# Optimization experiments

Measured on AMD Instinct MI355X. Metric: run time of the kernel, lower is better.

Reference implementation:

```python
import jax, jax.numpy as jnp
import numpy as np

N, E, H, FE, FV, L, FL, FO = 20000, 320000, 256, 64, 64, 4, 1024, 1


def setup_inputs() -> dict:
    key = jax.random.key(0)
    ks = jax.random.split(key, 28)
    s = 0.05
    rn = lambda k, shp: jax.random.normal(k, shp, jnp.float32) * s
    inp = {
        'x': jax.random.normal(ks[0], (N, FV), jnp.float32),
        'edge_attr': jax.random.normal(ks[1], (E, FE), jnp.float32),
        'edge_index': jax.random.randint(ks[2], (2, E), 0, N, jnp.int64) if False else jax.random.randint(ks[2], (2, E), 0, N),
        'ew': rn(ks[3], (H, FE)), 'eb': rn(ks[4], (H,)),
        'vw': rn(ks[5], (H, FV)), 'vb': rn(ks[6], (H,)),
        'Le_w': rn(ks[7], (L, H, H)), 'Le_b': rn(ks[8], (L, H)),
        'Lv_w': rn(ks[9], (L, H, H)), 'Lv_b': rn(ks[10], (L, H)),
        'bne_g': jnp.ones((L, H), jnp.float32), 'bne_b': jnp.zeros((L, H), jnp.float32),
        'bnv_g': jnp.ones((L, H), jnp.float32), 'bnv_b': jnp.zeros((L, H), jnp.float32),
        'gru_wih': rn(ks[11], (L, 3 * H, H)), 'gru_whh': rn(ks[12], (L, 3 * H, H)),
        'gru_bih': rn(ks[13], (L, 3 * H)), 'gru_bhh': rn(ks[14], (L, 3 * H)),
        'fin_w': rn(ks[15], (FL, H)), 'fin_b': rn(ks[16], (FL,)),
        'out_w': rn(ks[17], (FO, FL)), 'out_b': rn(ks[18], (FO,)),
    }
    return inp


def _bn(x, g, b):
    # BatchNorm1d, training-mode batch statistics (biased variance), eps=1e-5
    m = x.mean(axis=0)
    v = x.var(axis=0)
    return (x - m) * jax.lax.rsqrt(v + 1e-5) * g + b


def _forward(x, edge_attr, edge_index, ew, eb, vw, vb, Le_w, Le_b, Lv_w, Lv_b,
             bne_g, bne_b, bnv_g, bnv_b, gru_wih, gru_whh, gru_bih, gru_bhh,
             fin_w, fin_b, out_w, out_b):
    n_nodes = x.shape[0]
    num_layers = Le_w.shape[0]
    src, dst = edge_index[0], edge_index[1]
    seg = jnp.concatenate([src, dst])  # each edge contributes to both endpoints
    e_in = edge_attr @ ew.T + eb       # [E, H]
    v_in = x @ vw.T + vb               # [N, H]
    for k in range(num_layers):
        e = e_in @ Le_w[k].T + Le_b[k]
        vp = v_in @ Lv_w[k].T + Lv_b[k]
        ep = jax.nn.relu(_bn(e + vp[src] + vp[dst], bne_g[k], bne_b[k]))  # [E, H]
        # scatter-max of incident edge features into each vertex
        vie = jax.ops.segment_max(jnp.concatenate([ep, ep], axis=0), seg,
                                  num_segments=n_nodes)
        vie = jnp.where(jnp.isfinite(vie), vie, 0.0)  # isolated vertices -> 0
        # single-step GRU: input vie, hidden v_in
        gi = vie @ gru_wih[k].T + gru_bih[k]
        gh = v_in @ gru_whh[k].T + gru_bhh[k]
        ir, iz, ig = jnp.split(gi, 3, axis=1)
        hr, hz, hg = jnp.split(gh, 3, axis=1)
        r = jax.nn.sigmoid(ir + hr)
        z = jax.nn.sigmoid(iz + hz)
        n = jnp.tanh(ig + r * hg)
        h = (1.0 - z) * n + z * v_in
        v_c = jax.nn.relu(_bn(h, bnv_g[k], bnv_b[k]))
        v_in = v_c + v_in
        e_in = ep + e_in
    e_fin = e_in @ fin_w.T + fin_b
    return e_fin @ out_w.T + out_b  # [E, 1]


def reference(x, edge_attr, edge_index, ew, eb, vw, vb, Le_w, Le_b, Lv_w, Lv_b,
              bne_g, bne_b, bnv_g, bnv_b, gru_wih, gru_whh, gru_bih, gru_bhh,
              fin_w, fin_b, out_w, out_b):
    return _forward(x, edge_attr, edge_index, ew, eb, vw, vb, Le_w, Le_b, Lv_w,
                    Lv_b, bne_g, bne_b, bnv_g, bnv_b, gru_wih, gru_whh,
                    gru_bih, gru_bhh, fin_w, fin_b, out_w, out_b)
```

## Files before the change

kernel.cpp:

```cpp
#include <hip/hip_runtime.h>
#include <stdint.h>

constexpr int N  = 20000;
constexpr int E  = 320000;
constexpr int H  = 256;
constexpr int FEAT = 64;
constexpr int NL = 4;
constexpr int FL = 1024;
constexpr int NB_E = E / 64;

typedef unsigned short u16;
typedef short bf16x8 __attribute__((ext_vector_type(8)));
typedef float f32x4 __attribute__((ext_vector_type(4)));

__device__ __forceinline__ float bf2f(u16 u) {
    union { uint32_t i; float f; } v; v.i = ((uint32_t)u) << 16; return v.f;
}
__device__ __forceinline__ u16 f2bf(float f) {
    union { uint32_t i; float f; } v; v.f = f;
    uint32_t r = v.i + 0x7FFFu + ((v.i >> 16) & 1u);
    return (u16)(r >> 16);
}
__device__ __forceinline__ float sigmf(float x) { return 1.f / (1.f + __expf(-x)); }
__device__ __forceinline__ float tanhf_(float x) { return 2.f / (1.f + __expf(-2.f * x)) - 1.f; }

__device__ __forceinline__ unsigned int encf(float x) {
    unsigned int u = __float_as_uint(x);
    return (u & 0x80000000u) ? ~u : (u | 0x80000000u);
}
__device__ __forceinline__ float decf(unsigned int k) {
    unsigned int u = (k & 0x80000000u) ? (k ^ 0x80000000u) : ~k;
    return __uint_as_float(u);
}
__device__ __forceinline__ bf16x8 addbf8(bf16x8 a, bf16x8 b) {
    bf16x8 o;
#pragma unroll
    for (int j = 0; j < 8; ++j)
        o[j] = (short)f2bf(bf2f((u16)(unsigned short)a[j]) + bf2f((u16)(unsigned short)b[j]));
    return o;
}

template <bool W16>
__device__ __forceinline__ bf16x8 ldb(const u16* wb, const float* wf, size_t off) {
    if constexpr (W16) {
        return *(const bf16x8*)(wb + off);
    } else {
        float4 b0 = *(const float4*)(wf + off);
        float4 b1 = *(const float4*)(wf + off + 4);
        bf16x8 r;
        r[0] = (short)f2bf(b0.x); r[1] = (short)f2bf(b0.y);
        r[2] = (short)f2bf(b0.z); r[3] = (short)f2bf(b0.w);
        r[4] = (short)f2bf(b1.x); r[5] = (short)f2bf(b1.y);
        r[6] = (short)f2bf(b1.z); r[7] = (short)f2bf(b1.w);
        return r;
    }
}

__global__ void k_fuse_final(const float* __restrict__ fin_w, const float* __restrict__ fin_b,
                             const float* __restrict__ out_w, const float* __restrict__ out_b,
                             float* __restrict__ w_fo) {
    int h = threadIdx.x;
    float acc = 0.f;
    for (int f = 0; f < FL; ++f) acc = fmaf(out_w[f], fin_w[(size_t)f * H + h], acc);
    w_fo[h] = acc;
    if (h == 0) {
        float b = 0.f;
        for (int f = 0; f < FL; ++f) b = fmaf(out_w[f], fin_b[f], b);
        w_fo[H] = b + out_b[0];
    }
}

__global__ void k_cvt_w(const float* __restrict__ w, u16* __restrict__ o, int n4) {
    int i = blockIdx.x * 256 + threadIdx.x;
    if (i < n4) {
        float4 v = *(const float4*)(w + (size_t)i * 4);
        *(ushort4*)(o + (size_t)i * 4) = make_ushort4(f2bf(v.x), f2bf(v.y), f2bf(v.z), f2bf(v.w));
    }
}

__global__ void k_cvt_w_sw(const float* __restrict__ w, u16* __restrict__ o, int total) {
    int i = blockIdx.x * 256 + threadIdx.x;
    if (i >= total) return;
    int l16 = i & 15;
    int qd  = (i >> 4) & 3;
    int ks  = (i >> 6) & 7;
    int g   = (i >> 9) & 15;
    int ly  = i >> 13;
    int row = g * 16 + l16;
    int k   = ks * 32 + qd * 8;
    const float* src = w + ((size_t)ly * H + row) * H + k;
    u16* dst = o + (size_t)i * 8;
    *(ushort4*)dst       = make_ushort4(f2bf(src[0]), f2bf(src[1]), f2bf(src[2]), f2bf(src[3]));
    *(ushort4*)(dst + 4) = make_ushort4(f2bf(src[4]), f2bf(src[5]), f2bf(src[6]), f2bf(src[7]));
}

__global__ void k_zero_int(int* __restrict__ p, int n) {
    int i = blockIdx.x * 256 + threadIdx.x;
    if (i < n) p[i] = 0;
}
__global__ void k_zero_f64(double* __restrict__ p, int n) {
    int i = blockIdx.x * 256 + threadIdx.x;
    if (i < n) p[i] = 0.0;
}
__global__ void k_hist2(const int* __restrict__ src, const int* __restrict__ dst,
                        int* __restrict__ curS, int* __restrict__ curD) {
    int e = blockIdx.x * 256 + threadIdx.x;
    if (e < E) { atomicAdd(&curS[src[e]], 1); atomicAdd(&curD[dst[e]], 1); }
}
__global__ void k_scan(int* __restrict__ cur) {
    __shared__ int cs[256];
    int t = threadIdx.x;
    constexpr int CH = (N + 255) / 256;
    int beg = t * CH, end = min(beg + CH, N);
    int s = 0;
    for (int i = beg; i < end; ++i) s += cur[i];
    cs[t] = s;
    __syncthreads();
    for (int off = 1; off < 256; off <<= 1) {
        int v = cs[t];
        int u = (t >= off) ? cs[t - off] : 0;
        __syncthreads();
        cs[t] = v + u;
        __syncthreads();
    }
    int run = (t > 0) ? cs[t - 1] : 0;
    for (int i = beg; i < end; ++i) { int d = cur[i]; cur[i] = run; run += d; }
}
__global__ void k_fill_perm(const int* __restrict__ src, const int* __restrict__ dst,
                            int* __restrict__ curS, int* __restrict__ curD,
                            int4* __restrict__ adjS, int4* __restrict__ sd2, int* __restrict__ pos) {
    int e = blockIdx.x * 256 + threadIdx.x;
    if (e < E) {
        int s = src[e], d = dst[e];
        int q = atomicAdd(&curD[d], 1);
        sd2[q] = make_int4(s, d, e, 0);
        pos[e] = q;
        int p = atomicAdd(&curS[s], 1);
        adjS[p] = make_int4(q, s, d, s);
    }
}
__global__ void k_fill_u32(unsigned int* __restrict__ p, unsigned int val) {
    size_t i = ((size_t)blockIdx.x * 256 + threadIdx.x) * 4;
    uint4 v = make_uint4(val, val, val, val);
    *(uint4*)(p + i) = v;
}

template <bool W16>
__global__ __launch_bounds__(256, 3) void k_proj_mfma(
    const float* __restrict__ A, const u16* __restrict__ wb, const float* __restrict__ wf,
    const float* __restrict__ bias, u16* __restrict__ C, int M, const int* __restrict__ perm)
{
    __shared__ u16 As[64][72];
    int t = threadIdx.x;
    int row0 = blockIdx.x * 64;
    int r = t >> 2, q = t & 3;
    if (row0 + r < M) {
        const float* gp = A + (size_t)(row0 + r) * FEAT + q * 16;
#pragma unroll
        for (int i = 0; i < 4; ++i) {
            float4 v = *(const float4*)(gp + i * 4);
            *(ushort4*)&As[r][q * 16 + i * 4] = make_ushort4(f2bf(v.x), f2bf(v.y), f2bf(v.z), f2bf(v.w));
        }
    } else {
#pragma unroll
        for (int i = 0; i < 4; ++i) *(ushort4*)&As[r][q * 16 + i * 4] = make_ushort4(0, 0, 0, 0);
    }
    __syncthreads();
    int w = t >> 6, l = t & 63, lane16 = l & 15, quad = l >> 4;
    f32x4 acc[4][4];
#pragma unroll
    for (int i = 0; i < 4; ++i)
#pragma unroll
        for (int j = 0; j < 4; ++j) acc[i][j] = (f32x4){0.f, 0.f, 0.f, 0.f};
#pragma unroll
    for (int k0 = 0; k0 < FEAT; k0 += 32) {
        bf16x8 a[4], b[4];
#pragma unroll
        for (int mt = 0; mt < 4; ++mt)
            a[mt] = *(const bf16x8*)&As[mt * 16 + lane16][k0 + quad * 8];
#pragma unroll
        for (int nt = 0; nt < 4; ++nt)
            b[nt] = ldb<W16>(wb, wf, (size_t)(w * 16 + nt * 64 + lane16) * FEAT + k0 + quad * 8);
#pragma unroll
        for (int mt = 0; mt < 4; ++mt)
#pragma unroll
            for (int nt = 0; nt < 4; ++nt)
                acc[mt][nt] = __builtin_amdgcn_mfma_f32_16x16x32_bf16(a[mt], b[nt], acc[mt][nt], 0, 0, 0);
    }
#pragma unroll
    for (int nt = 0; nt < 4; ++nt) {
        int col = w * 16 + nt * 64 + lane16;
        float bv = bias[col];
#pragma unroll
        for (int mt = 0; mt < 4; ++mt)
#pragma unroll
            for (int reg = 0; reg < 4; ++reg) {
                int row = mt * 16 + quad * 4 + reg;
                if (row0 + row < M) {
                    int pr = perm ? perm[row0 + row] : row0 + row;
                    C[(size_t)pr * H + col] = f2bf(acc[mt][nt][reg] + bv);
                }
            }
    }
}

template <bool W16>
__global__ __launch_bounds__(256, 2) void k_node_mfma(
    const u16* __restrict__ A, const u16* __restrict__ wb, const float* __restrict__ wf,
    u16* __restrict__ C)
{
    __shared__ u16 As[64][264];
    int t = threadIdx.x;
    int row0 = blockIdx.x * 64;
    int rows = min(64, N - row0);
    int r = t >> 2, q = t & 3;
    if (r < rows) {
        const u16* gp = A + (size_t)(row0 + r) * H + q * 64;
#pragma unroll
        for (int i = 0; i < 16; ++i)
            *(ushort4*)&As[r][q * 64 + i * 4] = *(const ushort4*)(gp + i * 4);
    } else {
#pragma unroll
        for (int i = 0; i < 16; ++i) *(ushort4*)&As[r][q * 64 + i * 4] = make_ushort4(0, 0, 0, 0);
    }
    __syncthreads();
    int w = t >> 6, l = t & 63, lane16 = l & 15, quad = l >> 4;
    f32x4 acc[4][4];
#pragma unroll
    for (int i = 0; i < 4; ++i)
#pragma unroll
        for (int j = 0; j < 4; ++j) acc[i][j] = (f32x4){0.f, 0.f, 0.f, 0.f};
    for (int k0 = 0; k0 < H; k0 += 32) {
        bf16x8 a[4], b[4];
#pragma unroll
        for (int mt = 0; mt < 4; ++mt)
            a[mt] = *(const bf16x8*)&As[mt * 16 + lane16][k0 + quad * 8];
#pragma unroll
        for (int nt = 0; nt < 4; ++nt)
            b[nt] = ldb<W16>(wb, wf, (size_t)(w * 16 + nt * 64 + lane16) * H + k0 + quad * 8);
#pragma unroll
        for (int mt = 0; mt < 4; ++mt)
#pragma unroll
            for (int nt = 0; nt < 4; ++nt)
                acc[mt][nt] = __builtin_amdgcn_mfma_f32_16x16x32_bf16(a[mt], b[nt], acc[mt][nt], 0, 0, 0);
    }
#pragma unroll
    for (int nt = 0; nt < 4; ++nt) {
        int col = w * 16 + nt * 64 + lane16;
#pragma unroll
        for (int mt = 0; mt < 4; ++mt)
#pragma unroll
            for (int reg = 0; reg < 4; ++reg) {
                int row = mt * 16 + quad * 4 + reg;
                if (row < rows)
                    C[(size_t)(row0 + row) * H + col] = f2bf(acc[mt][nt][reg]);
            }
    }
}

__global__ __launch_bounds__(512, 4) void k_edge_first(
    const u16* __restrict__ ein2, const u16* __restrict__ wsw,
    const u16* __restrict__ vp, const int4* __restrict__ sd2,
    const int* __restrict__ endo,
    unsigned int* __restrict__ vie, double* __restrict__ stats_e)
{
    __shared__ u16 As[64][264];
    __shared__ u16 Us[64][264];
    __shared__ int s_node[64];
    __shared__ int s_int[64];
    u16 (*praw)[264] = As;

    int t = threadIdx.x;
    int p0 = blockIdx.x * 64;
    int r = t >> 3, q = t & 7;
    {
        int4 en = sd2[p0 + r];
        const u16* gp = ein2 + (size_t)(p0 + r) * H + q * 32;
        const u16* vs = vp + (size_t)en.x * H + q * 32;
        const u16* vd = vp + (size_t)en.y * H + q * 32;
#pragma unroll
        for (int i = 0; i < 4; ++i)
            *(bf16x8*)&As[r][q * 32 + i * 8] = *(const bf16x8*)(gp + i * 8);
#pragma unroll
        for (int i = 0; i < 4; ++i) {
            bf16x8 a8 = *(const bf16x8*)(vs + i * 8);
            bf16x8 b8 = *(const bf16x8*)(vd + i * 8);
            *(bf16x8*)&Us[r][q * 32 + i * 8] = addbf8(a8, b8);
        }
    }
    if (t < 64) {
        int nd = sd2[p0 + t].y;
        s_node[t] = nd;
        int seg0 = p0 + (t & 32);
        int st = (nd == 0) ? 0 : endo[nd - 1];
        int ee = endo[nd];
        s_int[t] = (st >= seg0) && (ee <= seg0 + 32);
    }
    __syncthreads();

    int w = t >> 6, l = t & 63, lane16 = l & 15, quad = l >> 4;
    f32x4 acc[4][2];
#pragma unroll
    for (int i = 0; i < 4; ++i)
#pragma unroll
        for (int j = 0; j < 2; ++j) acc[i][j] = (f32x4){0.f, 0.f, 0.f, 0.f};
    int woff = (quad * 16 + lane16) * 8;
    for (int ks = 0; ks < 8; ++ks) {
        int k0 = ks * 32;
        bf16x8 a[4], b[2];
#pragma unroll
        for (int mt = 0; mt < 4; ++mt)
            a[mt] = *(const bf16x8*)&As[mt * 16 + lane16][k0 + quad * 8];
#pragma unroll
        for (int nt = 0; nt < 2; ++nt)
            b[nt] = *(const bf16x8*)(wsw + (size_t)(w * 2 + nt) * 4096 + ks * 512 + woff);
#pragma unroll
        for (int mt = 0; mt < 4; ++mt)
#pragma unroll
            for (int nt = 0; nt < 2; ++nt)
                acc[mt][nt] = __builtin_amdgcn_mfma_f32_16x16x32_bf16(a[mt], b[nt], acc[mt][nt], 0, 0, 0);
    }
    __syncthreads();

#pragma unroll
    for (int nt = 0; nt < 2; ++nt) {
        int col = w * 32 + nt * 16 + lane16;
        float s = 0.f, qq = 0.f;
#pragma unroll
        for (int mt = 0; mt < 4; ++mt)
#pragma unroll
            for (int reg = 0; reg < 4; ++reg) {
                int row = mt * 16 + quad * 4 + reg;
                float v = acc[mt][nt][reg] + bf2f(Us[row][col]);
                praw[row][col] = f2bf(v);
                s += v; qq += v * v;
            }
        s  += __shfl_xor(s, 16, 64);  s  += __shfl_xor(s, 32, 64);
        qq += __shfl_xor(qq, 16, 64); qq += __shfl_xor(qq, 32, 64);
        if (quad == 0) {
            int slice = blockIdx.x & 63;
            atomicAdd(&stats_e[(size_t)slice * 512 + col], (double)s);
            atomicAdd(&stats_e[(size_t)slice * 512 + 256 + col], (double)qq);
        }
    }
    __syncthreads();
    {
        int seg = t >> 8, col = t & 255;
        int base = seg * 32;
        int cur = s_node[base];
        float m = bf2f(praw[base][col]);
        for (int rr = 1; rr < 32; ++rr) {
            int nd = s_node[base + rr];
            float v = bf2f(praw[base + rr][col]);
            if (nd != cur) {
                if (s_int[base + rr - 1]) vie[(size_t)cur * H + col] = encf(m);
                else atomicMax(&vie[(size_t)cur * H + col], encf(m));
                cur = nd; m = v;
            } else m = fmaxf(m, v);
        }
        if (s_int[base + 31]) vie[(size_t)cur * H + col] = encf(m);
        else atomicMax(&vie[(size_t)cur * H + col], encf(m));
    }
}

__global__ __launch_bounds__(512, 4) void k_edge_second(
    const u16* __restrict__ ein2, const u16* __restrict__ wsw,
    const u16* __restrict__ vp, const int4* __restrict__ adj,
    unsigned int* __restrict__ vie,
    const float* __restrict__ scale, const float* __restrict__ shift,
    u16* __restrict__ ein_rw)
{
    __shared__ u16 As[64][264];
    __shared__ u16 Us[64][264];
    __shared__ int s_pos[64];
    __shared__ int s_node[64];
    u16 (*praw)[264] = As;

    int t = threadIdx.x;
    int p0 = blockIdx.x * 64;
    int r = t >> 3, q = t & 7;
    {
        int4 en = adj[p0 + r];
        const u16* gp = ein2 + (size_t)en.x * H + q * 32;
        const u16* vs = vp + (size_t)en.y * H + q * 32;
        const u16* vd = vp + (size_t)en.z * H + q * 32;
#pragma unroll
        for (int i = 0; i < 4; ++i)
            *(bf16x8*)&As[r][q * 32 + i * 8] = *(const bf16x8*)(gp + i * 8);
#pragma unroll
        for (int i = 0; i < 4; ++i) {
            bf16x8 a8 = *(const bf16x8*)(vs + i * 8);
            bf16x8 b8 = *(const bf16x8*)(vd + i * 8);
            *(bf16x8*)&Us[r][q * 32 + i * 8] = addbf8(a8, b8);
        }
    }
    if (t < 64) {
        int4 en = adj[p0 + t];
        s_pos[t] = en.x; s_node[t] = en.w;
    }
    __syncthreads();

    int w = t >> 6, l = t & 63, lane16 = l & 15, quad = l >> 4;
    f32x4 acc[4][2];
#pragma unroll
    for (int i = 0; i < 4; ++i)
#pragma unroll
        for (int j = 0; j < 2; ++j) acc[i][j] = (f32x4){0.f, 0.f, 0.f, 0.f};
    int woff = (quad * 16 + lane16) * 8;
    for (int ks = 0; ks < 8; ++ks) {
        int k0 = ks * 32;
        bf16x8 a[4], b[2];
#pragma unroll
        for (int mt = 0; mt < 4; ++mt)
            a[mt] = *(const bf16x8*)&As[mt * 16 + lane16][k0 + quad * 8];
#pragma unroll
        for (int nt = 0; nt < 2; ++nt)
            b[nt] = *(const bf16x8*)(wsw + (size_t)(w * 2 + nt) * 4096 + ks * 512 + woff);
#pragma unroll
        for (int mt = 0; mt < 4; ++mt)
#pragma unroll
            for (int nt = 0; nt < 2; ++nt)
                acc[mt][nt] = __builtin_amdgcn_mfma_f32_16x16x32_bf16(a[mt], b[nt], acc[mt][nt], 0, 0, 0);
    }
    __syncthreads();

#pragma unroll
    for (int nt = 0; nt < 2; ++nt) {
        int col = w * 32 + nt * 16 + lane16;
#pragma unroll
        for (int mt = 0; mt < 4; ++mt)
#pragma unroll
            for (int reg = 0; reg < 4; ++reg) {
                int row = mt * 16 + quad * 4 + reg;
                praw[row][col] = f2bf(acc[mt][nt][reg] + bf2f(Us[row][col]));
            }
    }
    __syncthreads();
    {
        int seg = t >> 8, col = t & 255;
        int base = seg * 32;
        int cur = s_node[base];
        float m = bf2f(praw[base][col]);
        for (int rr = 1; rr < 32; ++rr) {
            int nd = s_node[base + rr];
            float v = bf2f(praw[base + rr][col]);
            if (nd != cur) {
                atomicMax(&vie[(size_t)cur * H + col], encf(m));
                cur = nd; m = v;
            } else m = fmaxf(m, v);
        }
        atomicMax(&vie[(size_t)cur * H + col], encf(m));
    }
    {
        u16* gp = ein_rw + (size_t)s_pos[r] * H + q * 32;
        const float* scp = scale + q * 32;
        const float* shp = shift + q * 32;
#pragma unroll
        for (int i = 0; i < 8; ++i) {
            int c = q * 32 + i * 4;
            ushort2 pa = *(const ushort2*)&praw[r][c];
            ushort2 pb = *(const ushort2*)&praw[r][c + 2];
            float4 sc = *(const float4*)(scp + i * 4);
            float4 sh = *(const float4*)(shp + i * 4);
            ushort4 ev = *(const ushort4*)(gp + i * 4);
            float o0 = bf2f(ev.x) + fmaxf(fmaf(bf2f(pa.x), sc.x, sh.x), 0.f);
            float o1 = bf2f(ev.y) + fmaxf(fmaf(bf2f(pa.y), sc.y, sh.y), 0.f);
            float o2 = bf2f(ev.z) + fmaxf(fmaf(bf2f(pb.x), sc.z, sh.z), 0.f);
            float o3 = bf2f(ev.w) + fmaxf(fmaf(bf2f(pb.y), sc.w, sh.w), 0.f);
            *(ushort4*)(gp + i * 4) = make_ushort4(f2bf(o0), f2bf(o1), f2bf(o2), f2bf(o3));
        }
    }
}

__global__ void k_bn_final_e(const double* __restrict__ stats_e,
                             const float* __restrict__ g, const float* __restrict__ b,
                             float* __restrict__ scale, float* __restrict__ shift) {
    int j = threadIdx.x;
    double m = 0.0, q = 0.0;
    for (int s = 0; s < 64; ++s) {
        m += stats_e[(size_t)s * 512 + j];
        q += stats_e[(size_t)s * 512 + 256 + j];
    }
    m /= (double)E;
    double var = q / (double)E - m * m;
    if (var < 0.0) var = 0.0;
    float inv = rsqrtf((float)var + 1e-5f);
    float sc = g[j] * inv;
    scale[j] = sc;
    shift[j] = b[j] - (float)m * sc;
}

__global__ void k_bn_final(const double* __restrict__ stats, int base,
                           const float* __restrict__ g, const float* __restrict__ b,
                           double cnt, float* __restrict__ scale, float* __restrict__ shift) {
    int j = threadIdx.x;
    double m = stats[base + j] / cnt;
    double var = stats[base + 256 + j] / cnt - m * m;
    if (var < 0.0) var = 0.0;
    float inv = rsqrtf((float)var + 1e-5f);
    float sc = g[j] * inv;
    scale[j] = sc;
    shift[j] = b[j] - (float)m * sc;
}

__global__ void k_vie_final(unsigned int* __restrict__ vie_u,
                            const float* __restrict__ scale, const float* __restrict__ shift) {
    size_t idx = ((size_t)blockIdx.x * 256 + threadIdx.x) * 4;
    int col = (int)(idx & (size_t)(H - 1));
    uint4 u = *(const uint4*)(vie_u + idx);
    float4 sc = *(const float4*)(scale + col);
    float4 sh = *(const float4*)(shift + col);
    float4 o;
    o.x = (u.x == 0u) ? 0.f : fmaxf(fmaf(decf(u.x), sc.x, sh.x), 0.f);
    o.y = (u.y == 0u) ? 0.f : fmaxf(fmaf(decf(u.y), sc.y, sh.y), 0.f);
    o.z = (u.z == 0u) ? 0.f : fmaxf(fmaf(decf(u.z), sc.z, sh.z), 0.f);
    o.w = (u.w == 0u) ? 0.f : fmaxf(fmaf(decf(u.w), sc.w, sh.w), 0.f);
    *(float4*)((float*)vie_u + idx) = o;
}

template <bool W16>
__global__ __launch_bounds__(256, 3) void k_gru_mfma(
    const float* __restrict__ vie, const u16* __restrict__ vin,
    const u16* __restrict__ wihb, const float* __restrict__ wihf,
    const u16* __restrict__ whhb, const float* __restrict__ whhf,
    const float* __restrict__ bih, const float* __restrict__ bhh,
    u16* __restrict__ hout, double* __restrict__ stats_v)
{
    __shared__ u16 Ae[32][264];
    __shared__ u16 Av[32][264];
    __shared__ float csum[256], csq[256];
    int t = threadIdx.x;
    int row0 = blockIdx.x * 32;
    int rows = min(32, N - row0);
    int r = t >> 3, q = t & 7;
    if (r < rows) {
        const float* gp = vie + (size_t)(row0 + r) * H + q * 32;
        const u16* hp = vin + (size_t)(row0 + r) * H + q * 32;
#pragma unroll
        for (int i = 0; i < 8; ++i) {
            float4 v = *(const float4*)(gp + i * 4);
            *(ushort4*)&Ae[r][q * 32 + i * 4] = make_ushort4(f2bf(v.x), f2bf(v.y), f2bf(v.z), f2bf(v.w));
        }
#pragma unroll
        for (int i = 0; i < 4; ++i)
            *(bf16x8*)&Av[r][q * 32 + i * 8] = *(const bf16x8*)(hp + i * 8);
    } else {
#pragma unroll
        for (int i = 0; i < 8; ++i) {
            *(ushort4*)&Ae[r][q * 32 + i * 4] = make_ushort4(0, 0, 0, 0);
            *(ushort4*)&Av[r][q * 32 + i * 4] = make_ushort4(0, 0, 0, 0);
        }
    }
    __syncthreads();
    int w = t >> 6, l = t & 63, lane16 = l & 15, quad = l >> 4;

    for (int g = 0; g < 4; ++g) {
        int j = g * 64 + w * 16 + lane16;
        f32x4 aR[2], aZ[2], aIG[2], aHG[2];
#pragma unroll
        for (int mt = 0; mt < 2; ++mt) {
            aR[mt] = (f32x4){0.f, 0.f, 0.f, 0.f};  aZ[mt] = (f32x4){0.f, 0.f, 0.f, 0.f};
            aIG[mt] = (f32x4){0.f, 0.f, 0.f, 0.f}; aHG[mt] = (f32x4){0.f, 0.f, 0.f, 0.f};
        }
        for (int k0 = 0; k0 < H; k0 += 32) {
            size_t kq = (size_t)k0 + quad * 8;
            bf16x8 ae[2], av[2];
#pragma unroll
            for (int mt = 0; mt < 2; ++mt) {
                ae[mt] = *(const bf16x8*)&Ae[mt * 16 + lane16][k0 + quad * 8];
                av[mt] = *(const bf16x8*)&Av[mt * 16 + lane16][k0 + quad * 8];
            }
            bf16x8 bri = ldb<W16>(wihb, wihf, (size_t)j * H + kq);
            bf16x8 bzi = ldb<W16>(wihb, wihf, (size_t)(H + j) * H + kq);
            bf16x8 bgi = ldb<W16>(wihb, wihf, (size_t)(2 * H + j) * H + kq);
            bf16x8 brh = ldb<W16>(whhb, whhf, (size_t)j * H + kq);
            bf16x8 bzh = ldb<W16>(whhb, whhf, (size_t)(H + j) * H + kq);
            bf16x8 bgh = ldb<W16>(whhb, whhf, (size_t)(2 * H + j) * H + kq);
#pragma unroll
            for (int mt = 0; mt < 2; ++mt) {
                aR[mt]  = __builtin_amdgcn_mfma_f32_16x16x32_bf16(ae[mt], bri, aR[mt], 0, 0, 0);
                aR[mt]  = __builtin_amdgcn_mfma_f32_16x16x32_bf16(av[mt], brh, aR[mt], 0, 0, 0);
                aZ[mt]  = __builtin_amdgcn_mfma_f32_16x16x32_bf16(ae[mt], bzi, aZ[mt], 0, 0, 0);
                aZ[mt]  = __builtin_amdgcn_mfma_f32_16x16x32_bf16(av[mt], bzh, aZ[mt], 0, 0, 0);
                aIG[mt] = __builtin_amdgcn_mfma_f32_16x16x32_bf16(ae[mt], bgi, aIG[mt], 0, 0, 0);
                aHG[mt] = __builtin_amdgcn_mfma_f32_16x16x32_bf16(av[mt], bgh, aHG[mt], 0, 0, 0);
            }
        }
        float br_ = bih[j] + bhh[j];
        float bz_ = bih[H + j] + bhh[H + j];
        float bgi_ = bih[2 * H + j];
        float bgh_ = bhh[2 * H + j];
        float s = 0.f, qq = 0.f;
#pragma unroll
        for (int mt = 0; mt < 2; ++mt)
#pragma unroll
            for (int reg = 0; reg < 4; ++reg) {
                int row = mt * 16 + quad * 4 + reg;
                float rr = sigmf(aR[mt][reg] + br_);
                float zz = sigmf(aZ[mt][reg] + bz_);
                float nn = tanhf_(aIG[mt][reg] + bgi_ + rr * (aHG[mt][reg] + bgh_));
                float vv = bf2f(Av[row][j]);
                float hv = (1.f - zz) * nn + zz * vv;
                if (row < rows) {
                    hout[(size_t)(row0 + row) * H + j] = f2bf(hv);
                    s += hv; qq += hv * hv;
                }
            }
        s  += __shfl_xor(s, 16, 64);  s  += __shfl_xor(s, 32, 64);
        qq += __shfl_xor(qq, 16, 64); qq += __shfl_xor(qq, 32, 64);
        if (quad == 0) { csum[j] = s; csq[j] = qq; }
    }
    __syncthreads();
    atomicAdd(&stats_v[t], (double)csum[t]);
    atomicAdd(&stats_v[256 + t], (double)csq[t]);
}

__global__ void k_vertex_update(u16* __restrict__ vin, const u16* __restrict__ h,
                                const float* __restrict__ scale, const float* __restrict__ shift) {
    size_t idx = ((size_t)blockIdx.x * 256 + threadIdx.x) * 4;
    int col = (int)(idx & (size_t)(H - 1));
    ushort4 hv = *(const ushort4*)(h + idx);
    float4 sc = *(const float4*)(scale + col);
    float4 sh = *(const float4*)(shift + col);
    ushort4 vv = *(const ushort4*)(vin + idx);
    float o0 = bf2f(vv.x) + fmaxf(fmaf(bf2f(hv.x), sc.x, sh.x), 0.f);
    float o1 = bf2f(vv.y) + fmaxf(fmaf(bf2f(hv.y), sc.y, sh.y), 0.f);
    float o2 = bf2f(vv.z) + fmaxf(fmaf(bf2f(hv.z), sc.z, sh.z), 0.f);
    float o3 = bf2f(vv.w) + fmaxf(fmaf(bf2f(hv.w), sc.w, sh.w), 0.f);
    *(ushort4*)(vin + idx) = make_ushort4(f2bf(o0), f2bf(o1), f2bf(o2), f2bf(o3));
}

__global__ __launch_bounds__(256) void k_final(const u16* __restrict__ ein2,
                                               const int4* __restrict__ sd2,
                                               const float* __restrict__ w_fo, float* __restrict__ out) {
    int t = threadIdx.x;
    int lane = t & 63;
    int w = (blockIdx.x << 2) + (t >> 6);
    float4 wv = *(const float4*)(w_fo + lane * 4);
    float bfo = w_fo[H];
    int p0 = w * 64;
    for (int p = p0; p < p0 + 64; ++p) {
        ushort4 u = *(const ushort4*)(ein2 + (size_t)p * H + lane * 4);
        float s = bf2f(u.x) * wv.x + bf2f(u.y) * wv.y + bf2f(u.z) * wv.z + bf2f(u.w) * wv.w;
        for (int off = 32; off > 0; off >>= 1) s += __shfl_down(s, off, 64);
        if (lane == 0) out[sd2[p].z] = s + bfo;
    }
}

template <bool W16>
static void run_all(void* const* d_in, void* d_out, void* d_ws, hipStream_t stream) {
    const float* x         = (const float*)d_in[0];
    const float* edge_attr = (const float*)d_in[1];
    const int*   ei        = (const int*)d_in[2];
    const int*   src = ei;
    const int*   dst = ei + E;
    const float* ew  = (const float*)d_in[3];
    const float* eb  = (const float*)d_in[4];
    const float* vw  = (const float*)d_in[5];
    const float* vb  = (const float*)d_in[6];
    const float* Le_w = (const float*)d_in[7];
    const float* Lv_w = (const float*)d_in[9];
    const float* bne_g = (const float*)d_in[11];
    const float* bne_b = (const float*)d_in[12];
    const float* bnv_g = (const float*)d_in[13];
    const float* bnv_b = (const float*)d_in[14];
    const float* gwih  = (const float*)d_in[15];
    const float* gwhh  = (const float*)d_in[16];
    const float* gbih  = (const float*)d_in[17];
    const float* gbhh  = (const float*)d_in[18];
    const float* fin_w = (const float*)d_in[19];
    const float* fin_b = (const float*)d_in[20];
    const float* out_w = (const float*)d_in[21];
    const float* out_b = (const float*)d_in[22];
    float* out = (float*)d_out;

    const size_t nh = (size_t)N * H, eh = (size_t)E * H;
    char* base = (char*)d_ws;
    size_t off = 0;
    auto alloc = [&](size_t bytes) -> char* {
        char* p = base + off;
        off = (off + bytes + 255) & ~(size_t)255;
        return p;
    };
    float* w_fo = (float*)alloc((H + 1) * sizeof(float));
    u16* v_in = (u16*)alloc(nh * sizeof(u16));
    u16* vp   = (u16*)alloc(nh * sizeof(u16));
    unsigned int* vie_u = (unsigned int*)alloc(nh * sizeof(unsigned int));
    u16* e_in = (u16*)alloc(eh * sizeof(u16));
    u16* wbf  = (u16*)alloc((size_t)NL * H * H * sizeof(u16));
    double* stats_e = (double*)alloc((size_t)64 * 512 * sizeof(double));
    double* stats_v = (double*)alloc(512 * sizeof(double));
    float* scale_e = (float*)alloc(H * sizeof(float));
    float* shift_e = (float*)alloc(H * sizeof(float));
    float* scale_v = (float*)alloc(H * sizeof(float));
    float* shift_v = (float*)alloc(H * sizeof(float));
    int* curS = (int*)alloc((size_t)N * sizeof(int));
    int* curD = (int*)alloc((size_t)N * sizeof(int));
    int4* adjS = (int4*)alloc((size_t)E * sizeof(int4));
    int4* sd2  = (int4*)alloc((size_t)E * sizeof(int4));
    int*  pos  = (int*)alloc((size_t)E * sizeof(int));
    u16 *wbf_v = nullptr, *wbf_ih = nullptr, *wbf_hh = nullptr, *ew_b = nullptr, *vw_b = nullptr;
    if (W16) {
        wbf_v  = (u16*)alloc((size_t)NL * H * H * sizeof(u16));
        wbf_ih = (u16*)alloc((size_t)NL * 3 * H * H * sizeof(u16));
        wbf_hh = (u16*)alloc((size_t)NL * 3 * H * H * sizeof(u16));
        ew_b   = (u16*)alloc((size_t)H * FEAT * sizeof(u16));
        vw_b   = (u16*)alloc((size_t)H * FEAT * sizeof(u16));
    }
    u16* hbuf = vp;

    k_fuse_final<<<1, 256, 0, stream>>>(fin_w, fin_b, out_w, out_b, w_fo);
    k_cvt_w_sw<<<(NL * H * H / 8 + 255) / 256, 256, 0, stream>>>(Le_w, wbf, NL * H * H / 8);
    if (W16) {
        k_cvt_w<<<(NL * H * H / 4 + 255) / 256, 256, 0, stream>>>(Lv_w, wbf_v, NL * H * H / 4);
        k_cvt_w<<<(NL * 3 * H * H / 4 + 255) / 256, 256, 0, stream>>>(gwih, wbf_ih, NL * 3 * H * H / 4);
        k_cvt_w<<<(NL * 3 * H * H / 4 + 255) / 256, 256, 0, stream>>>(gwhh, wbf_hh, NL * 3 * H * H / 4);
        k_cvt_w<<<(H * FEAT / 4 + 255) / 256, 256, 0, stream>>>(ew, ew_b, H * FEAT / 4);
        k_cvt_w<<<(H * FEAT / 4 + 255) / 256, 256, 0, stream>>>(vw, vw_b, H * FEAT / 4);
    }
    k_zero_int<<<(N + 255) / 256, 256, 0, stream>>>(curS, N);
    k_zero_int<<<(N + 255) / 256, 256, 0, stream>>>(curD, N);
    k_hist2<<<E / 256, 256, 0, stream>>>(src, dst, curS, curD);
    k_scan<<<1, 256, 0, stream>>>(curS);
    k_scan<<<1, 256, 0, stream>>>(curD);
    k_fill_perm<<<E / 256, 256, 0, stream>>>(src, dst, curS, curD, adjS, sd2, pos);
    const int ntile = (N + 63) / 64;
    k_proj_mfma<W16><<<ntile, 256, 0, stream>>>(x, vw_b, vw, vb, v_in, N, nullptr);
    k_proj_mfma<W16><<<E / 64, 256, 0, stream>>>(edge_attr, ew_b, ew, eb, e_in, E, pos);

    const int nstat = 64 * 512 + 512;
    const int gtile = (N + 31) / 32;
    for (int k = 0; k < NL; ++k) {
        k_zero_f64<<<(nstat + 255) / 256, 256, 0, stream>>>(stats_e, nstat);
        k_fill_u32<<<(int)(nh / 4 / 256), 256, 0, stream>>>(vie_u, 0u);
        k_node_mfma<W16><<<ntile, 256, 0, stream>>>(v_in,
            W16 ? wbf_v + (size_t)k * H * H : nullptr, Lv_w + (size_t)k * H * H, vp);
        k_edge_first<<<NB_E, 512, 0, stream>>>(e_in, wbf + (size_t)k * H * H, vp,
                                               sd2, curD, vie_u, stats_e);
        k_bn_final_e<<<1, 256, 0, stream>>>(stats_e, bne_g + k * H, bne_b + k * H, scale_e, shift_e);
        k_edge_second<<<NB_E, 512, 0, stream>>>(e_in, wbf + (size_t)k * H * H, vp,
                                                adjS, vie_u, scale_e, shift_e, e_in);
        k_vie_final<<<(int)(nh / 4 / 256), 256, 0, stream>>>(vie_u, scale_e, shift_e);
        k_gru_mfma<W16><<<gtile, 256, 0, stream>>>((const float*)vie_u, v_in,
            W16 ? wbf_ih + (size_t)k * 3 * H * H : nullptr, gwih + (size_t)k * 3 * H * H,
            W16 ? wbf_hh + (size_t)k * 3 * H * H : nullptr, gwhh + (size_t)k * 3 * H * H,
            gbih + (size_t)k * 3 * H, gbhh + (size_t)k * 3 * H, hbuf, stats_v);
        k_bn_final<<<1, 256, 0, stream>>>(stats_v, 0, bnv_g + k * H, bnv_b + k * H, (double)N, scale_v, shift_v);
        k_vertex_update<<<(int)(nh / 4 / 256), 256, 0, stream>>>(v_in, hbuf, scale_v, shift_v);
    }
    k_final<<<E / 256, 256, 0, stream>>>(e_in, sd2, w_fo, out);
}

extern "C" void kernel_launch(void* const* d_in, const int* in_sizes, int n_in,
                              void* d_out, int out_size, void* d_ws, size_t ws_size,
                              hipStream_t stream) {
    (void)in_sizes; (void)n_in; (void)out_size;
    const size_t nh = (size_t)N * H, eh = (size_t)E * H;
    auto rup = [](size_t x) { return (x + 255) & ~(size_t)255; };
    size_t need_base = rup((H + 1) * 4) + 2 * rup(nh * 2) + rup(nh * 4) + rup(eh * 2)
                     + rup((size_t)NL * H * H * 2) + rup((size_t)64 * 512 * 8) + rup(512 * 8)
                     + 4 * rup(H * 4) + 2 * rup((size_t)N * 4) + 2 * rup((size_t)E * 16)
                     + rup((size_t)E * 4);
    size_t need_w16 = rup((size_t)NL * H * H * 2)
                    + 2 * rup((size_t)NL * 3 * H * H * 2) + 2 * rup((size_t)H * FEAT * 2);
    if (ws_size == 0 || ws_size >= need_base + need_w16)
        run_all<true>(d_in, d_out, d_ws, stream);
    else
        run_all<false>(d_in, d_out, d_ws, stream);
}
```

Before: 2.444 ms.

## Pre-swizzle all bf16 weights into MFMA fragment order for coalesced loads

Result: no change. 2.467 ms (median of 3 runs) (+1.0%).

```diff
diff --git a/kernel.cpp b/kernel.cpp
--- a/kernel.cpp
+++ b/kernel.cpp
@@ -40,20 +40,15 @@
     return o;
 }
 
-template <bool W16>
-__device__ __forceinline__ bf16x8 ldb(const u16* wb, const float* wf, size_t off) {
-    if constexpr (W16) {
-        return *(const bf16x8*)(wb + off);
-    } else {
-        float4 b0 = *(const float4*)(wf + off);
-        float4 b1 = *(const float4*)(wf + off + 4);
-        bf16x8 r;
-        r[0] = (short)f2bf(b0.x); r[1] = (short)f2bf(b0.y);
-        r[2] = (short)f2bf(b0.z); r[3] = (short)f2bf(b0.w);
-        r[4] = (short)f2bf(b1.x); r[5] = (short)f2bf(b1.y);
-        r[6] = (short)f2bf(b1.z); r[7] = (short)f2bf(b1.w);
-        return r;
-    }
+__device__ __forceinline__ bf16x8 ldbf(const float* wf, size_t off) {
+    float4 b0 = *(const float4*)(wf + off);
+    float4 b1 = *(const float4*)(wf + off + 4);
+    bf16x8 r;
+    r[0] = (short)f2bf(b0.x); r[1] = (short)f2bf(b0.y);
+    r[2] = (short)f2bf(b0.z); r[3] = (short)f2bf(b0.w);
+    r[4] = (short)f2bf(b1.x); r[5] = (short)f2bf(b1.y);
+    r[6] = (short)f2bf(b1.z); r[7] = (short)f2bf(b1.w);
+    return r;
 }
 
 __global__ void k_fuse_final(const float* __restrict__ fin_w, const float* __restrict__ fin_b,
@@ -70,25 +65,18 @@
     }
 }
 
-__global__ void k_cvt_w(const float* __restrict__ w, u16* __restrict__ o, int n4) {
-    int i = blockIdx.x * 256 + threadIdx.x;
-    if (i < n4) {
-        float4 v = *(const float4*)(w + (size_t)i * 4);
-        *(ushort4*)(o + (size_t)i * 4) = make_ushort4(f2bf(v.x), f2bf(v.y), f2bf(v.z), f2bf(v.w));
-    }
-}
-
-__global__ void k_cvt_w_sw(const float* __restrict__ w, u16* __restrict__ o, int total) {
+__global__ void k_cvt_frag(const float* __restrict__ w, u16* __restrict__ o,
+                           int R, int K, int total) {
     int i = blockIdx.x * 256 + threadIdx.x;
     if (i >= total) return;
-    int l16 = i & 15;
-    int qd  = (i >> 4) & 3;
-    int ks  = (i >> 6) & 7;
-    int g   = (i >> 9) & 15;
-    int ly  = i >> 13;
-    int row = g * 16 + l16;
-    int k   = ks * 32 + qd * 8;
-    const float* src = w + ((size_t)ly * H + row) * H + k;
+    int fpm = (R * K) >> 3;
+    int m = i / fpm, f = i % fpm;
+    int l16 = f & 15, qd = (f >> 4) & 3;
+    int rem = f >> 6;
+    int kdiv = K >> 5;
+    int ks = rem % kdiv, g = rem / kdiv;
+    int row = g * 16 + l16, k = ks * 32 + qd * 8;
+    const float* src = w + ((size_t)m * R + row) * K + k;
     u16* dst = o + (size_t)i * 8;
     *(ushort4*)dst       = make_ushort4(f2bf(src[0]), f2bf(src[1]), f2bf(src[2]), f2bf(src[3]));
     *(ushort4*)(dst + 4) = make_ushort4(f2bf(src[4]), f2bf(src[5]), f2bf(src[6]), f2bf(src[7]));
@@ -172,15 +160,21 @@
     for (int i = 0; i < 4; ++i)
 #pragma unroll
         for (int j = 0; j < 4; ++j) acc[i][j] = (f32x4){0.f, 0.f, 0.f, 0.f};
+    int foff = (quad * 16 + lane16) * 8;
 #pragma unroll
     for (int k0 = 0; k0 < FEAT; k0 += 32) {
+        int ks = k0 >> 5;
         bf16x8 a[4], b[4];
 #pragma unroll
         for (int mt = 0; mt < 4; ++mt)
             a[mt] = *(const bf16x8*)&As[mt * 16 + lane16][k0 + quad * 8];
 #pragma unroll
-        for (int nt = 0; nt < 4; ++nt)
-            b[nt] = ldb<W16>(wb, wf, (size_t)(w * 16 + nt * 64 + lane16) * FEAT + k0 + quad * 8);
+        for (int nt = 0; nt < 4; ++nt) {
+            if constexpr (W16)
+                b[nt] = *(const bf16x8*)(wb + (size_t)((nt * 4 + w) * 2 + ks) * 512 + foff);
+            else
+                b[nt] = ldbf(wf, (size_t)(w * 16 + nt * 64 + lane16) * FEAT + k0 + quad * 8);
+        }
 #pragma unroll
         for (int mt = 0; mt < 4; ++mt)
 #pragma unroll
@@ -217,8 +211,8 @@
     if (r < rows) {
         const u16* gp = A + (size_t)(row0 + r) * H + q * 64;
 #pragma unroll
-        for (int i = 0; i < 16; ++i)
-            *(ushort4*)&As[r][q * 64 + i * 4] = *(const ushort4*)(gp + i * 4);
+        for (int i = 0; i < 8; ++i)
+            *(bf16x8*)&As[r][q * 64 + i * 8] = *(const bf16x8*)(gp + i * 8);
     } else {
 #pragma unroll
         for (int i = 0; i < 16; ++i) *(ushort4*)&As[r][q * 64 + i * 4] = make_ushort4(0, 0, 0, 0);
@@ -230,14 +224,20 @@
     for (int i = 0; i < 4; ++i)
 #pragma unroll
         for (int j = 0; j < 4; ++j) acc[i][j] = (f32x4){0.f, 0.f, 0.f, 0.f};
+    int foff = (quad * 16 + lane16) * 8;
     for (int k0 = 0; k0 < H; k0 += 32) {
+        int ks = k0 >> 5;
         bf16x8 a[4], b[4];
 #pragma unroll
         for (int mt = 0; mt < 4; ++mt)
             a[mt] = *(const bf16x8*)&As[mt * 16 + lane16][k0 + quad * 8];
 #pragma unroll
-        for (int nt = 0; nt < 4; ++nt)
-            b[nt] = ldb<W16>(wb, wf, (size_t)(w * 16 + nt * 64 + lane16) * H + k0 + quad * 8);
+        for (int nt = 0; nt < 4; ++nt) {
+            if constexpr (W16)
+                b[nt] = *(const bf16x8*)(wb + (size_t)((nt * 4 + w) * 8 + ks) * 512 + foff);
+            else
+                b[nt] = ldbf(wf, (size_t)(w * 16 + nt * 64 + lane16) * H + k0 + quad * 8);
+        }
 #pragma unroll
         for (int mt = 0; mt < 4; ++mt)
 #pragma unroll
@@ -379,14 +379,17 @@
     int t = threadIdx.x;
     int p0 = blockIdx.x * 64;
     int r = t >> 3, q = t & 7;
+    bf16x8 ein_reg[4];
     {
         int4 en = adj[p0 + r];
         const u16* gp = ein2 + (size_t)en.x * H + q * 32;
         const u16* vs = vp + (size_t)en.y * H + q * 32;
         const u16* vd = vp + (size_t)en.z * H + q * 32;
 #pragma unroll
-        for (int i = 0; i < 4; ++i)
-            *(bf16x8*)&As[r][q * 32 + i * 8] = *(const bf16x8*)(gp + i * 8);
+        for (int i = 0; i < 4; ++i) {
+            ein_reg[i] = *(const bf16x8*)(gp + i * 8);
+            *(bf16x8*)&As[r][q * 32 + i * 8] = ein_reg[i];
+        }
 #pragma unroll
         for (int i = 0; i < 4; ++i) {
             bf16x8 a8 = *(const bf16x8*)(vs + i * 8);
@@ -456,18 +459,19 @@
         const float* scp = scale + q * 32;
         const float* shp = shift + q * 32;
 #pragma unroll
-        for (int i = 0; i < 8; ++i) {
-            int c = q * 32 + i * 4;
-            ushort2 pa = *(const ushort2*)&praw[r][c];
-            ushort2 pb = *(const ushort2*)&praw[r][c + 2];
-            float4 sc = *(const float4*)(scp + i * 4);
-            float4 sh = *(const float4*)(shp + i * 4);
-            ushort4 ev = *(const ushort4*)(gp + i * 4);
-            float o0 = bf2f(ev.x) + fmaxf(fmaf(bf2f(pa.x), sc.x, sh.x), 0.f);
-            float o1 = bf2f(ev.y) + fmaxf(fmaf(bf2f(pa.y), sc.y, sh.y), 0.f);
-            float o2 = bf2f(ev.z) + fmaxf(fmaf(bf2f(pb.x), sc.z, sh.z), 0.f);
-            float o3 = bf2f(ev.w) + fmaxf(fmaf(bf2f(pb.y), sc.w, sh.w), 0.f);
-            *(ushort4*)(gp + i * 4) = make_ushort4(f2bf(o0), f2bf(o1), f2bf(o2), f2bf(o3));
+        for (int i = 0; i < 4; ++i) {
+            int c = q * 32 + i * 8;
+            bf16x8 pr = *(const bf16x8*)&praw[r][c];
+            bf16x8 ov;
+#pragma unroll
+            for (int j = 0; j < 8; ++j) {
+                float sc = scp[i * 8 + j];
+                float sh = shp[i * 8 + j];
+                float o = bf2f((u16)(unsigned short)ein_reg[i][j])
+                        + fmaxf(fmaf(bf2f((u16)(unsigned short)pr[j]), sc, sh), 0.f);
+                ov[j] = (short)f2bf(o);
+            }
+            *(bf16x8*)(gp + i * 8) = ov;
         }
     }
 }
@@ -553,6 +557,7 @@
     }
     __syncthreads();
     int w = t >> 6, l = t & 63, lane16 = l & 15, quad = l >> 4;
+    int foff = (quad * 16 + lane16) * 8;
 
     for (int g = 0; g < 4; ++g) {
         int j = g * 64 + w * 16 + lane16;
@@ -563,19 +568,30 @@
             aIG[mt] = (f32x4){0.f, 0.f, 0.f, 0.f}; aHG[mt] = (f32x4){0.f, 0.f, 0.f, 0.f};
         }
         for (int k0 = 0; k0 < H; k0 += 32) {
-            size_t kq = (size_t)k0 + quad * 8;
             bf16x8 ae[2], av[2];
 #pragma unroll
             for (int mt = 0; mt < 2; ++mt) {
                 ae[mt] = *(const bf16x8*)&Ae[mt * 16 + lane16][k0 + quad * 8];
                 av[mt] = *(const bf16x8*)&Av[mt * 16 + lane16][k0 + quad * 8];
             }
-            bf16x8 bri = ldb<W16>(wihb, wihf, (size_t)j * H + kq);
-            bf16x8 bzi = ldb<W16>(wihb, wihf, (size_t)(H + j) * H + kq);
-            bf16x8 bgi = ldb<W16>(wihb, wihf, (size_t)(2 * H + j) * H + kq);
-            bf16x8 brh = ldb<W16>(whhb, whhf, (size_t)j * H + kq);
-            bf16x8 bzh = ldb<W16>(whhb, whhf, (size_t)(H + j) * H + kq);
-            bf16x8 bgh = ldb<W16>(whhb, whhf, (size_t)(2 * H + j) * H + kq);
+            bf16x8 bri, bzi, bgi, brh, bzh, bgh;
+            if constexpr (W16) {
+                size_t fo = ((size_t)(g * 4 + w) * 8 + (k0 >> 5)) * 512 + foff;
+                bri = *(const bf16x8*)(wihb + fo);
+                bzi = *(const bf16x8*)(wihb + 65536 + fo);
+                bgi = *(const bf16x8*)(wihb + 131072 + fo);
+                brh = *(const bf16x8*)(whhb + fo);
+                bzh = *(const bf16x8*)(whhb + 65536 + fo);
+                bgh = *(const bf16x8*)(whhb + 131072 + fo);
+            } else {
+                size_t kq = (size_t)k0 + quad * 8;
+                bri = ldbf(wihf, (size_t)j * H + kq);
+                bzi = ldbf(wihf, (size_t)(H + j) * H + kq);
+                bgi = ldbf(wihf, (size_t)(2 * H + j) * H + kq);
+                brh = ldbf(whhf, (size_t)j * H + kq);
+                bzh = ldbf(whhf, (size_t)(H + j) * H + kq);
+                bgh = ldbf(whhf, (size_t)(2 * H + j) * H + kq);
+            }
 #pragma unroll
             for (int mt = 0; mt < 2; ++mt) {
                 aR[mt]  = __builtin_amdgcn_mfma_f32_16x16x32_bf16(ae[mt], bri, aR[mt], 0, 0, 0);
@@ -710,13 +726,13 @@
     u16* hbuf = vp;
 
     k_fuse_final<<<1, 256, 0, stream>>>(fin_w, fin_b, out_w, out_b, w_fo);
-    k_cvt_w_sw<<<(NL * H * H / 8 + 255) / 256, 256, 0, stream>>>(Le_w, wbf, NL * H * H / 8);
+    k_cvt_frag<<<(NL * H * H / 8 + 255) / 256, 256, 0, stream>>>(Le_w, wbf, H, H, NL * H * H / 8);
     if (W16) {
-        k_cvt_w<<<(NL * H * H / 4 + 255) / 256, 256, 0, stream>>>(Lv_w, wbf_v, NL * H * H / 4);
-        k_cvt_w<<<(NL * 3 * H * H / 4 + 255) / 256, 256, 0, stream>>>(gwih, wbf_ih, NL * 3 * H * H / 4);
-        k_cvt_w<<<(NL * 3 * H * H / 4 + 255) / 256, 256, 0, stream>>>(gwhh, wbf_hh, NL * 3 * H * H / 4);
-        k_cvt_w<<<(H * FEAT / 4 + 255) / 256, 256, 0, stream>>>(ew, ew_b, H * FEAT / 4);
-        k_cvt_w<<<(H * FEAT / 4 + 255) / 256, 256, 0, stream>>>(vw, vw_b, H * FEAT / 4);
+        k_cvt_frag<<<(NL * H * H / 8 + 255) / 256, 256, 0, stream>>>(Lv_w, wbf_v, H, H, NL * H * H / 8);
+        k_cvt_frag<<<(NL * 3 * H * H / 8 + 255) / 256, 256, 0, stream>>>(gwih, wbf_ih, H, H, NL * 3 * H * H / 8);
+        k_cvt_frag<<<(NL * 3 * H * H / 8 + 255) / 256, 256, 0, stream>>>(gwhh, wbf_hh, H, H, NL * 3 * H * H / 8);
+        k_cvt_frag<<<(H * FEAT / 8 + 255) / 256, 256, 0, stream>>>(ew, ew_b, H, FEAT, H * FEAT / 8);
+        k_cvt_frag<<<(H * FEAT / 8 + 255) / 256, 256, 0, stream>>>(vw, vw_b, H, FEAT, H * FEAT / 8);
     }
     k_zero_int<<<(N + 255) / 256, 256, 0, stream>>>(curS, N);
     k_zero_int<<<(N + 255) / 256, 256, 0, stream>>>(curD, N);
```
